# Performance work log

Hardware: AMD Instinct MI355X
Metric: run time of the kernel (lower is better)

The kernel has to match this reference:

```python
import jax, jax.numpy as jnp
import numpy as np

WS = 14   # window_size
NH = 12   # num_heads

def _rel_index(ws):
    # Deterministic relative-position index buffer, identical to the torch module.
    coords = np.stack(np.meshgrid(np.arange(ws), np.arange(ws), indexing='ij'))  # [2,ws,ws]
    cf = coords.reshape(2, -1)                                                   # [2,N]
    rel = (cf[:, :, None] - cf[:, None, :]).transpose(1, 2, 0).astype(np.int64)  # [N,N,2]
    rel[..., 0] += ws - 1
    rel[..., 1] += ws - 1
    rel[..., 0] *= 2 * ws - 1
    return rel.sum(-1)  # [N,N]


def setup_inputs() -> dict:
    key = jax.random.key(0)
    ks = jax.random.split(key, 5)
    B, H, W, C = 16, 56, 56, 768
    x = jax.random.normal(ks[0], (B, H * W, C), jnp.float32)
    qkv_w = jax.random.normal(ks[1], (3 * C, C), jnp.float32) * 0.02
    q_bias = jnp.zeros((C,), jnp.float32)
    v_bias = jnp.zeros((C,), jnp.float32)
    rel_bias_table = jax.random.normal(ks[2], ((2 * WS - 1) ** 2, NH), jnp.float32) * 0.02
    proj_w = jax.random.normal(ks[3], (C, C), jnp.float32) * 0.02
    proj_b = jnp.zeros((C,), jnp.float32)
    return {"x": x, "qkv_w": qkv_w, "q_bias": q_bias, "v_bias": v_bias,
            "rel_bias_table": rel_bias_table, "proj_w": proj_w, "proj_b": proj_b,
            "H": H, "W": W}


def reference(x, qkv_w, q_bias, v_bias, rel_bias_table, proj_w, proj_b, H, W):
    B, L, C = x.shape
    ws, nh = WS, NH
    hd = C // nh
    scale = hd ** (-0.5)
    N = ws * ws

    # --- window partition with pad (H_, W_ are Python ints -> static) ---
    xs = x.reshape(B, H, W, C)
    H_ = -(-H // ws) * ws
    W_ = -(-W // ws) * ws
    xs = jnp.pad(xs, ((0, 0), (0, H_ - H), (0, W_ - W), (0, 0)))
    xw = xs.reshape(B, H_ // ws, ws, W_ // ws, ws, C).transpose(0, 1, 3, 2, 4, 5)
    xw = xw.reshape(-1, N, C)  # [Bw, N, C]

    # --- qkv with q/v bias (k bias is zero) ---
    qkv_b = jnp.concatenate([q_bias, jnp.zeros_like(v_bias), v_bias])
    qkv = (xw @ qkv_w.T + qkv_b).reshape(-1, N, 3, nh, hd).transpose(2, 0, 3, 1, 4)
    q, k, v = qkv[0] * scale, qkv[1], qkv[2]  # each [Bw, nh, N, hd]

    # --- scores + gathered relative-position bias + softmax ---
    attn = jnp.einsum('bhnd,bhmd->bhnm', q, k)
    idx = jnp.asarray(_rel_index(ws).reshape(-1))
    rpb = rel_bias_table[idx].reshape(N, N, nh).transpose(2, 0, 1)  # [nh,N,N]
    attn = jax.nn.softmax(attn + rpb[None], axis=-1)

    out = jnp.einsum('bhnm,bhmd->bhnd', attn, v).transpose(0, 2, 1, 3).reshape(-1, N, C)
    out = out @ proj_w.T + proj_b

    # --- window reverse + crop ---
    out = out.reshape(B, H_ // ws, W_ // ws, ws, ws, C).transpose(0, 1, 3, 2, 4, 5)
    out = out.reshape(B, H_, W_, C)[:, :H, :W, :].reshape(B, H * W, C)
    return out
```

## Files before the change

### kernel.cpp

```cpp
#include <hip/hip_runtime.h>

typedef unsigned short u16;
typedef unsigned int   u32;
typedef __bf16  bf16x8 __attribute__((ext_vector_type(8)));
typedef float   f32x4  __attribute__((ext_vector_type(4)));
typedef u16     u16x8  __attribute__((ext_vector_type(8)));
typedef u16     u16x4  __attribute__((ext_vector_type(4)));

__device__ __forceinline__ float bf2f(u16 v) {
    union { u32 i; float f; } u; u.i = (u32)v << 16; return u.f;
}
__device__ __forceinline__ u16 f2bf(float f) {
    union { float f; u32 i; } u; u.f = f;
    u32 r = (u.i + 0x7FFFu + ((u.i >> 16) & 1u)) >> 16;
    return (u16)r;
}
__device__ __forceinline__ bf16x8 ld8(const u16* p) {
    return __builtin_bit_cast(bf16x8, *(const u16x8*)p);
}
__device__ __forceinline__ void gload16(const void* g, void* l) {
    __builtin_amdgcn_global_load_lds((__attribute__((address_space(1))) void*)g,
                                     (__attribute__((address_space(3))) void*)l, 16, 0, 0);
}

__global__ void detect_kernel(const u16* __restrict__ x, int* __restrict__ flag) {
    if (threadIdx.x == 0 && blockIdx.x == 0) {
        int plausible = 0;
        for (int j = 0; j < 64; j++) {
            float a = fabsf(bf2f(x[2 * j]));
            if (a >= 0.0009765625f && a <= 16.0f) plausible++;
        }
        *flag = (plausible >= 32) ? 0 : 1;
    }
}

__global__ __launch_bounds__(256) void convert_kernel(
    const void* __restrict__ src, u16* __restrict__ dst, int n,
    const int* __restrict__ flag)
{
    int fp32 = *flag;
    int stride = gridDim.x * 256 * 4;
    for (int i = (blockIdx.x * 256 + threadIdx.x) * 4; i < n; i += stride) {
        if (fp32) {
            float4 v = *(const float4*)((const float*)src + i);
            u16x4 o = { f2bf(v.x), f2bf(v.y), f2bf(v.z), f2bf(v.w) };
            *(u16x4*)(dst + i) = o;
        } else {
            *(u16x4*)(dst + i) = *(const u16x4*)((const u16*)src + i);
        }
    }
}

__global__ __launch_bounds__(256) void rpb_prep(const u16* __restrict__ table,
                                                u16* __restrict__ RPB) {
    int idx = blockIdx.x * 256 + threadIdx.x;
    if (idx >= 12 * 13 * 13 * 256) return;
    int r  = idx & 15;
    int c  = (idx >> 4) & 15;
    int q  = idx >> 8;
    int tn = q % 13;
    int q2 = q / 13;
    int tm = q2 % 13;
    int h  = q2 / 13;
    int m = tm * 16 + r, n = tn * 16 + c;
    float val;
    if (n >= 196) {
        val = -30000.0f;
    } else {
        int mc = m > 195 ? 195 : m;
        int i1 = mc / 14, j1 = mc % 14, i2 = n / 14, j2 = n % 14;
        int t = (i1 - i2 + 13) * 27 + (j1 - j2 + 13);
        val = bf2f(table[t * 12 + h]);
    }
    RPB[idx] = f2bf(val);
}

template <int MODE, int NCOLS>
__global__ __launch_bounds__(512, 2) void gemm_kernel(
    const u16* __restrict__ A, const u16* __restrict__ Bw,
    const u16* __restrict__ bias0, const u16* __restrict__ bias1,
    void* __restrict__ Cc, const int* __restrict__ flag)
{
    __shared__ __align__(16) u16 lds[65536];

    const int tid  = threadIdx.x;
    const int wave = tid >> 6, lane = tid & 63;
    const int quad = lane >> 4, l16 = lane & 15;
    const int wr = wave >> 2, wc = wave & 3;

    const int nwg = gridDim.x;
    const int qq = nwg >> 3, rr = nwg & 7;
    const int xcd = blockIdx.x & 7, sub = blockIdx.x >> 3;
    const int wgid = (xcd < rr ? xcd * (qq + 1)
                               : rr * (qq + 1) + (xcd - rr) * qq) + sub;
    const int NT  = NCOLS / 256;
    const int bmt = wgid / NT;
    const int bnt = wgid - bmt * NT;
    const int bm  = bmt * 256, bn = bnt * 256;

    const int uA0 = tid, uA1 = tid + 512;
    const int rA0 = uA0 >> 2, rA1 = uA1 >> 2;
    const int cA0 = (uA0 & 3) ^ ((uA0 >> 3) & 3);
    const int cA1 = (uA1 & 3) ^ ((uA1 >> 3) & 3);
    const u16* gA0 = A  + (size_t)(bm + rA0) * 768 + cA0 * 8;
    const u16* gA1 = A  + (size_t)(bm + rA1) * 768 + cA1 * 8;
    const u16* gB0 = Bw + (size_t)(bn + rA0) * 768 + cA0 * 8;
    const u16* gB1 = Bw + (size_t)(bn + rA1) * 768 + cA1 * 8;
    char* ldsb = (char*)lds;

    const int cp   = quad ^ ((l16 >> 1) & 3);
    const int offA = ((wr * 128 + l16) * 4 + cp) * 8;
    const int offB = ((wc *  64 + l16) * 4 + cp) * 8 + 32768;

#define STAGE_A(tt, ss) do {                                                  \
    char* b_ = ldsb + (ss) * 16384 + wave * 1024;                             \
    gload16(gA0 + (tt) * 32, b_);                                             \
    gload16(gA1 + (tt) * 32, b_ + 8192); } while (0)
#define STAGE_B(tt, ss) do {                                                  \
    char* b_ = ldsb + 65536 + (ss) * 16384 + wave * 1024;                     \
    gload16(gB0 + (tt) * 32, b_);                                             \
    gload16(gB1 + (tt) * 32, b_ + 8192); } while (0)

    STAGE_A(0, 0); STAGE_B(0, 0);
    STAGE_A(1, 1); STAGE_B(1, 1);
    STAGE_A(2, 2); STAGE_B(2, 2);

    f32x4 acc[8][4] = {};
    bf16x8 afr[4], bfr[4];

#define TILE(t, VMC, DOSTAGE) do {                                            \
    asm volatile("s_waitcnt vmcnt(" #VMC ")" ::: "memory");                   \
    __builtin_amdgcn_s_barrier();                                             \
    asm volatile("" ::: "memory");                                            \
    const u16* sa = lds + ((t) & 3) * 8192;                                   \
    _Pragma("unroll") for (int n = 0; n < 4; n++)                             \
        bfr[n] = ld8(sa + offB + n * 512);                                    \
    _Pragma("unroll") for (int m = 0; m < 4; m++)                             \
        afr[m] = ld8(sa + offA + m * 512);                                    \
    if (DOSTAGE) STAGE_A((t) + 3, ((t) + 3) & 3);                             \
    __builtin_amdgcn_s_setprio(1);                                            \
    _Pragma("unroll") for (int m = 0; m < 4; m++)                             \
      _Pragma("unroll") for (int n = 0; n < 4; n++)                           \
        acc[m][n] = __builtin_amdgcn_mfma_f32_16x16x32_bf16(                  \
            afr[m], bfr[n], acc[m][n], 0, 0, 0);                              \
    __builtin_amdgcn_s_setprio(0);                                            \
    __builtin_amdgcn_s_barrier();                                             \
    _Pragma("unroll") for (int m = 0; m < 4; m++)                             \
        afr[m] = ld8(sa + offA + (m + 4) * 512);                              \
    if (DOSTAGE) STAGE_B((t) + 3, ((t) + 3) & 3);                             \
    __builtin_amdgcn_s_setprio(1);                                            \
    _Pragma("unroll") for (int m = 0; m < 4; m++)                             \
      _Pragma("unroll") for (int n = 0; n < 4; n++)                           \
        acc[m + 4][n] = __builtin_amdgcn_mfma_f32_16x16x32_bf16(              \
            afr[m], bfr[n], acc[m + 4][n], 0, 0, 0);                          \
    __builtin_amdgcn_s_setprio(0);                                            \
} while (0)

    for (int t = 0; t < 21; ++t) TILE(t, 8, 1);
    TILE(21, 8, 0);
    TILE(22, 4, 0);
    TILE(23, 0, 0);

#undef TILE
#undef STAGE_A
#undef STAGE_B

    __syncthreads();

    float bs[4], scl[4];
#pragma unroll
    for (int n = 0; n < 4; n++) {
        int col = bn + wc * 64 + n * 16 + l16;
        if (MODE == 0) {
            if (col < 768)       { bs[n] = bf2f(bias0[col]);        scl[n] = 0.125f; }
            else if (col < 1536) { bs[n] = 0.f;                     scl[n] = 1.f; }
            else                 { bs[n] = bf2f(bias1[col - 1536]); scl[n] = 1.f; }
        } else {
            bs[n] = bf2f(bias0[col]); scl[n] = 1.f;
        }
    }
    const int fp32out = (MODE == 1) ? *flag : 0;
    u16* scratch = &lds[wave * 2048];

#pragma unroll
    for (int m = 0; m < 8; m++) {
#pragma unroll
        for (int n = 0; n < 4; n++)
#pragma unroll
            for (int r2 = 0; r2 < 4; r2++)
                scratch[(quad * 4 + r2) * 72 + n * 16 + l16] =
                    f2bf((acc[m][n][r2] + bs[n]) * scl[n]);
        asm volatile("s_waitcnt lgkmcnt(0)" ::: "memory");
#pragma unroll
        for (int j = 0; j < 2; j++) {
            int unit = j * 64 + lane;
            int row = unit >> 3, c8 = unit & 7;
            u16x8 val = *(const u16x8*)&scratch[row * 72 + c8 * 8];
            int gm = bm + wr * 128 + m * 16 + row;
            int gn = bn + wc * 64 + c8 * 8;
            size_t off;
            if (MODE == 0) {
                off = (size_t)gm * NCOLS + gn;
            } else {
                int wwin = gm / 196, tt = gm % 196;
                int b2 = wwin >> 4, wh2 = (wwin >> 2) & 3, ww2 = wwin & 3;
                int ti = tt / 14, tj = tt % 14;
                int g = b2 * 3136 + (wh2 * 14 + ti) * 56 + ww2 * 14 + tj;
                off = (size_t)g * NCOLS + gn;
            }
            if (MODE == 1 && fp32out) {
                float* outf = (float*)Cc;
                float4 lo = { bf2f(val[0]), bf2f(val[1]), bf2f(val[2]), bf2f(val[3]) };
                float4 hi = { bf2f(val[4]), bf2f(val[5]), bf2f(val[6]), bf2f(val[7]) };
                *(float4*)&outf[off]     = lo;
                *(float4*)&outf[off + 4] = hi;
            } else {
                *(u16x8*)&((u16*)Cc)[off] = val;
            }
        }
    }
}

__global__ __launch_bounds__(256) void attn_kernel(
    const u16* __restrict__ QKV, const u16* __restrict__ RPB, u16* __restrict__ O)
{
    __shared__ __align__(16) u16 k_s[208][72];
    __shared__ __align__(16) u16 v_t[64][224];
    __shared__ __align__(16) u16 p_s[4][16][40];

    const int tid  = threadIdx.x;
    const int wave = tid >> 6, lane = tid & 63;
    const int quad = lane >> 4, l16 = lane & 15;
    const int w = blockIdx.x / 12, h = blockIdx.x % 12;
    const int b = w >> 4, wh = (w >> 2) & 3, ww = w & 3;
    const int gbase = b * 3136 + wh * 14 * 56 + ww * 14;

    for (int c = tid; c < 1568; c += 256) {
        int tok = c >> 3, dg = c & 7;
        int ti = tok / 14, tj = tok % 14;
        size_t grow = (size_t)(gbase + ti * 56 + tj) * 2304 + h * 64 + dg * 8;
        uint4 kk = *(const uint4*)&QKV[grow + 768];
        *(uint4*)&k_s[tok][dg * 8] = kk;
        uint4 vv = *(const uint4*)&QKV[grow + 1536];
        const u16* pv = (const u16*)&vv;
#pragma unroll
        for (int j = 0; j < 8; j++) v_t[dg * 8 + j][tok] = pv[j];
    }
    for (int c = tid; c < 12 * 64; c += 256) k_s[196 + (c >> 6)][c & 63] = 0;
    for (int c = tid; c < 64 * 28; c += 256) v_t[c / 28][196 + c % 28] = 0;
    __syncthreads();

    for (int tm = wave; tm < 13; tm += 4) {
        int tq = tm * 16 + l16; if (tq > 195) tq = 195;
        int qi = tq / 14, qj = tq % 14;
        size_t qoff = (size_t)(gbase + qi * 56 + qj) * 2304 + h * 64 + quad * 8;
        bf16x8 aq0 = ld8(&QKV[qoff]);
        bf16x8 aq1 = ld8(&QKV[qoff + 32]);

        f32x4 sc[13];
#pragma unroll
        for (int tn = 0; tn < 13; tn++) {
            bf16x8 bk0 = ld8(&k_s[tn * 16 + l16][quad * 8]);
            bf16x8 bk1 = ld8(&k_s[tn * 16 + l16][32 + quad * 8]);
            f32x4 z = {};
            z = __builtin_amdgcn_mfma_f32_16x16x32_bf16(aq0, bk0, z, 0, 0, 0);
            sc[tn] = __builtin_amdgcn_mfma_f32_16x16x32_bf16(aq1, bk1, z, 0, 0, 0);
        }
#pragma unroll
        for (int tn = 0; tn < 13; tn++) {
            const u16* rp = &RPB[((((h * 13 + tm) * 13 + tn) * 16 + l16) << 4) + quad * 4];
#pragma unroll
            for (int r = 0; r < 4; r++) sc[tn][r] += bf2f(rp[r]);
        }
        float inv[4];
#pragma unroll
        for (int r = 0; r < 4; r++) {
            float m = -3.0e38f;
#pragma unroll
            for (int tn = 0; tn < 13; tn++) m = fmaxf(m, sc[tn][r]);
#pragma unroll
            for (int d = 1; d < 16; d <<= 1) m = fmaxf(m, __shfl_xor(m, d, 64));
            float s = 0.f;
#pragma unroll
            for (int tn = 0; tn < 13; tn++) {
                float e = __expf(sc[tn][r] - m);
                sc[tn][r] = e; s += e;
            }
#pragma unroll
            for (int d = 1; d < 16; d <<= 1) s += __shfl_xor(s, d, 64);
            inv[r] = 1.f / s;
        }
        f32x4 oc[4] = {};
#pragma unroll
        for (int s7 = 0; s7 < 7; s7++) {
#pragma unroll
            for (int tt = 0; tt < 2; tt++) {
                int tn = 2 * s7 + tt;
#pragma unroll
                for (int r = 0; r < 4; r++) {
                    float pv = (tn < 13) ? sc[tn][r] * inv[r] : 0.f;
                    p_s[wave][quad * 4 + r][tt * 16 + l16] = f2bf(pv);
                }
            }
            __asm__ volatile("s_waitcnt lgkmcnt(0)" ::: "memory");
            bf16x8 ap = ld8(&p_s[wave][l16][quad * 8]);
#pragma unroll
            for (int dt = 0; dt < 4; dt++) {
                bf16x8 bv = ld8(&v_t[dt * 16 + l16][s7 * 32 + quad * 8]);
                oc[dt] = __builtin_amdgcn_mfma_f32_16x16x32_bf16(ap, bv, oc[dt], 0, 0, 0);
            }
        }
#pragma unroll
        for (int dt = 0; dt < 4; dt++)
#pragma unroll
            for (int r = 0; r < 4; r++) {
                int t = tm * 16 + quad * 4 + r;
                if (t < 196)
                    O[(size_t)(w * 196 + t) * 768 + h * 64 + dt * 16 + l16] = f2bf(oc[dt][r]);
            }
    }
}

extern "C" void kernel_launch(void* const* d_in, const int* in_sizes, int n_in,
                              void* d_out, int out_size, void* d_ws, size_t ws_size,
                              hipStream_t stream) {
    char* ws = (char*)d_ws;
    u16* qkv     = (u16*)(ws);
    u16* xbf     = (u16*)(ws + 231211008);
    u16* attnout = xbf;
    u16* wqkv_bf = (u16*)(ws + 308281344);
    u16* wproj_bf= (u16*)(ws + 311820288);
    u16* rpb     = (u16*)(ws + 312999936);
    u16* qb_bf   = (u16*)(ws + 314038272);
    u16* vb_bf   = (u16*)(ws + 314039808);
    u16* pb_bf   = (u16*)(ws + 314041344);
    u16* tbl_bf  = (u16*)(ws + 314042880);
    int* flag    = (int*)(ws + 314060384);

    detect_kernel<<<1, 64, 0, stream>>>((const u16*)d_in[0], flag);
    convert_kernel<<<4096, 256, 0, stream>>>(d_in[0], xbf,      16 * 3136 * 768, flag);
    convert_kernel<<<1728, 256, 0, stream>>>(d_in[1], wqkv_bf,  2304 * 768,      flag);
    convert_kernel<<< 576, 256, 0, stream>>>(d_in[5], wproj_bf, 768 * 768,       flag);
    convert_kernel<<<   1, 256, 0, stream>>>(d_in[2], qb_bf,    768,             flag);
    convert_kernel<<<   1, 256, 0, stream>>>(d_in[3], vb_bf,    768,             flag);
    convert_kernel<<<   1, 256, 0, stream>>>(d_in[6], pb_bf,    768,             flag);
    convert_kernel<<<   9, 256, 0, stream>>>(d_in[4], tbl_bf,   729 * 12,        flag);

    rpb_prep<<<2028, 256, 0, stream>>>(tbl_bf, rpb);
    gemm_kernel<0, 2304><<<dim3(1764), 512, 0, stream>>>(
        xbf, wqkv_bf, qb_bf, vb_bf, qkv, flag);
    attn_kernel<<<3072, 256, 0, stream>>>(qkv, rpb, attnout);
    gemm_kernel<1, 768><<<dim3(588), 512, 0, stream>>>(
        attnout, wproj_bf, pb_bf, pb_bf, d_out, flag);
}
```

Baseline: 712.2 us.

## Transpose score MFMA, swizzle V^T in LDS, batch P writes for attention

The QK^T MFMA operands are swapped so each lane holds a whole query row's scores. Softmax then reduces mostly in registers with two cross-lane shuffles instead of four per row, and the RPB prep layout is transposed to match. V^T in LDS gets an XOR swizzle and a padded stride to reduce bank conflicts. P tiles are written as packed 4-element stores in two batches with fewer waitcnt barriers. The detect kernel is also parallelised with a ballot. This adds LDS (a larger p_s) and relies on the swizzle indexing being consistent between the write and read sides.

Measured after the change: 715.4 us. About the same (+0.5%).

```diff
diff --git a/kernel.cpp b/kernel.cpp
--- a/kernel.cpp
+++ b/kernel.cpp
@@ -24,14 +24,11 @@
 }
 
 __global__ void detect_kernel(const u16* __restrict__ x, int* __restrict__ flag) {
-    if (threadIdx.x == 0 && blockIdx.x == 0) {
-        int plausible = 0;
-        for (int j = 0; j < 64; j++) {
-            float a = fabsf(bf2f(x[2 * j]));
-            if (a >= 0.0009765625f && a <= 16.0f) plausible++;
-        }
-        *flag = (plausible >= 32) ? 0 : 1;
-    }
+    int j = threadIdx.x;
+    float a = fabsf(bf2f(x[2 * j]));
+    int ok = (a >= 0.0009765625f && a <= 16.0f) ? 1 : 0;
+    unsigned long long m = __ballot(ok);
+    if (j == 0) *flag = (__popcll(m) >= 32) ? 0 : 1;
 }
 
 __global__ __launch_bounds__(256) void convert_kernel(
@@ -62,13 +59,13 @@
     int q2 = q / 13;
     int tm = q2 % 13;
     int h  = q2 / 13;
-    int m = tm * 16 + r, n = tn * 16 + c;
+    int kk = tn * 16 + r, qv = tm * 16 + c;
     float val;
-    if (n >= 196) {
+    if (kk >= 196) {
         val = -30000.0f;
     } else {
-        int mc = m > 195 ? 195 : m;
-        int i1 = mc / 14, j1 = mc % 14, i2 = n / 14, j2 = n % 14;
+        int qc = qv > 195 ? 195 : qv;
+        int i1 = qc / 14, j1 = qc % 14, i2 = kk / 14, j2 = kk % 14;
         int t = (i1 - i2 + 13) * 27 + (j1 - j2 + 13);
         val = bf2f(table[t * 12 + h]);
     }
@@ -225,8 +222,8 @@
     const u16* __restrict__ QKV, const u16* __restrict__ RPB, u16* __restrict__ O)
 {
     __shared__ __align__(16) u16 k_s[208][72];
-    __shared__ __align__(16) u16 v_t[64][224];
-    __shared__ __align__(16) u16 p_s[4][16][40];
+    __shared__ __align__(16) u16 v_t[64][232];
+    __shared__ __align__(16) u16 p_s[4][16][136];
 
     const int tid  = threadIdx.x;
     const int wave = tid >> 6, lane = tid & 63;
@@ -243,11 +240,15 @@
         *(uint4*)&k_s[tok][dg * 8] = kk;
         uint4 vv = *(const uint4*)&QKV[grow + 1536];
         const u16* pv = (const u16*)&vv;
-#pragma unroll
-        for (int j = 0; j < 8; j++) v_t[dg * 8 + j][tok] = pv[j];
+        int tsw = tok ^ ((dg & 3) << 3);
+#pragma unroll
+        for (int j = 0; j < 8; j++) v_t[dg * 8 + j][tsw] = pv[j];
     }
     for (int c = tid; c < 12 * 64; c += 256) k_s[196 + (c >> 6)][c & 63] = 0;
-    for (int c = tid; c < 64 * 28; c += 256) v_t[c / 28][196 + c % 28] = 0;
+    for (int c = tid; c < 64 * 28; c += 256) {
+        int row = c / 28, tok = 196 + c % 28;
+        v_t[row][tok ^ (((row >> 3) & 3) << 3)] = 0;
+    }
     __syncthreads();
 
     for (int tm = wave; tm < 13; tm += 4) {
@@ -263,8 +264,8 @@
             bf16x8 bk0 = ld8(&k_s[tn * 16 + l16][quad * 8]);
             bf16x8 bk1 = ld8(&k_s[tn * 16 + l16][32 + quad * 8]);
             f32x4 z = {};
-            z = __builtin_amdgcn_mfma_f32_16x16x32_bf16(aq0, bk0, z, 0, 0, 0);
-            sc[tn] = __builtin_amdgcn_mfma_f32_16x16x32_bf16(aq1, bk1, z, 0, 0, 0);
+            z = __builtin_amdgcn_mfma_f32_16x16x32_bf16(bk0, aq0, z, 0, 0, 0);
+            sc[tn] = __builtin_amdgcn_mfma_f32_16x16x32_bf16(bk1, aq1, z, 0, 0, 0);
         }
 #pragma unroll
         for (int tn = 0; tn < 13; tn++) {
@@ -272,42 +273,52 @@
 #pragma unroll
             for (int r = 0; r < 4; r++) sc[tn][r] += bf2f(rp[r]);
         }
-        float inv[4];
-#pragma unroll
-        for (int r = 0; r < 4; r++) {
-            float m = -3.0e38f;
-#pragma unroll
-            for (int tn = 0; tn < 13; tn++) m = fmaxf(m, sc[tn][r]);
-#pragma unroll
-            for (int d = 1; d < 16; d <<= 1) m = fmaxf(m, __shfl_xor(m, d, 64));
-            float s = 0.f;
-#pragma unroll
-            for (int tn = 0; tn < 13; tn++) {
-                float e = __expf(sc[tn][r] - m);
+        float mx = -3.0e38f;
+#pragma unroll
+        for (int tn = 0; tn < 13; tn++)
+#pragma unroll
+            for (int r = 0; r < 4; r++) mx = fmaxf(mx, sc[tn][r]);
+        mx = fmaxf(mx, __shfl_xor(mx, 16, 64));
+        mx = fmaxf(mx, __shfl_xor(mx, 32, 64));
+        float s = 0.f;
+#pragma unroll
+        for (int tn = 0; tn < 13; tn++)
+#pragma unroll
+            for (int r = 0; r < 4; r++) {
+                float e = __expf(sc[tn][r] - mx);
                 sc[tn][r] = e; s += e;
             }
-#pragma unroll
-            for (int d = 1; d < 16; d <<= 1) s += __shfl_xor(s, d, 64);
-            inv[r] = 1.f / s;
-        }
+        s += __shfl_xor(s, 16, 64);
+        s += __shfl_xor(s, 32, 64);
+        float invs = 1.f / s;
+
         f32x4 oc[4] = {};
 #pragma unroll
-        for (int s7 = 0; s7 < 7; s7++) {
-#pragma unroll
-            for (int tt = 0; tt < 2; tt++) {
-                int tn = 2 * s7 + tt;
-#pragma unroll
-                for (int r = 0; r < 4; r++) {
-                    float pv = (tn < 13) ? sc[tn][r] * inv[r] : 0.f;
-                    p_s[wave][quad * 4 + r][tt * 16 + l16] = f2bf(pv);
+        for (int g = 0; g < 2; g++) {
+            const int c0 = g ? 4 : 0;
+            const int cn = g ? 3 : 4;
+#pragma unroll
+            for (int ss = 0; ss < cn; ss++)
+#pragma unroll
+                for (int tt = 0; tt < 2; tt++) {
+                    int tn = 2 * (c0 + ss) + tt;
+                    u16x4 pk;
+#pragma unroll
+                    for (int r = 0; r < 4; r++)
+                        pk[r] = (tn < 13) ? f2bf(sc[tn][r] * invs) : (u16)0;
+                    *(u16x4*)&p_s[wave][l16][ss * 32 + tt * 16 + quad * 4] = pk;
                 }
-            }
-            __asm__ volatile("s_waitcnt lgkmcnt(0)" ::: "memory");
-            bf16x8 ap = ld8(&p_s[wave][l16][quad * 8]);
-#pragma unroll
-            for (int dt = 0; dt < 4; dt++) {
-                bf16x8 bv = ld8(&v_t[dt * 16 + l16][s7 * 32 + quad * 8]);
-                oc[dt] = __builtin_amdgcn_mfma_f32_16x16x32_bf16(ap, bv, oc[dt], 0, 0, 0);
+            asm volatile("s_waitcnt lgkmcnt(0)" ::: "memory");
+#pragma unroll
+            for (int ss = 0; ss < cn; ss++) {
+                int s7 = c0 + ss;
+                bf16x8 ap = ld8(&p_s[wave][l16][ss * 32 + quad * 8]);
+#pragma unroll
+                for (int dt = 0; dt < 4; dt++) {
+                    int xg = quad ^ ((2 * dt + (l16 >> 3)) & 3);
+                    bf16x8 bv = ld8(&v_t[dt * 16 + l16][s7 * 32 + xg * 8]);
+                    oc[dt] = __builtin_amdgcn_mfma_f32_16x16x32_bf16(ap, bv, oc[dt], 0, 0, 0);
+                }
             }
         }
 #pragma unroll
```
